# Kernel optimization log

Hardware: AMD Instinct MI355X
Metric: run time of the kernel (lower is better)

## Reference

```python
import jax, jax.numpy as jnp
import numpy as np

V, D, H, L, F, S, B = 32000, 1024, 16, 6, 4096, 1024, 2
DK = D // H
SCALE = float(np.sqrt(DK))
NEG = -1e9


def _make_pe(max_len, d_model):
    pos = np.arange(max_len, dtype=np.float32)[:, None]
    div = np.exp(np.arange(0, d_model, 2, dtype=np.float32) * (-np.log(10000.0) / d_model))
    pe = np.zeros((max_len, d_model), dtype=np.float32)
    pe[:, 0::2] = np.sin(pos * div)
    pe[:, 1::2] = np.cos(pos * div)
    return jnp.asarray(pe)


def _ln(x, g, b, eps=1e-5):
    m = x.mean(-1, keepdims=True)
    v = ((x - m) ** 2).mean(-1, keepdims=True)
    return (x - m) / jnp.sqrt(v + eps) * g + b


def setup_inputs() -> dict:
    key = jax.random.key(0)
    ks = jax.random.split(key, 10)
    std = 0.02
    tokens = jax.random.randint(ks[0], (B, S), 0, V)
    emb = (jax.random.normal(ks[1], (V, D)) * std).at[0].set(0.0)  # padding_idx=0 row zeroed
    pe = _make_pe(4096, D)
    Wq = jax.random.normal(ks[2], (L, D, D)) * std
    Wk = jax.random.normal(ks[3], (L, D, D)) * std
    Wv = jax.random.normal(ks[4], (L, D, D)) * std
    Wo = jax.random.normal(ks[5], (L, D, D)) * std
    bo = jnp.zeros((L, D))
    g1 = jnp.ones((L, D)); be1 = jnp.zeros((L, D))
    g2 = jnp.ones((L, D)); be2 = jnp.zeros((L, D))
    W1 = jax.random.normal(ks[6], (L, D, F)) * std
    b1 = jnp.zeros((L, F))
    W2 = jax.random.normal(ks[7], (L, F, D)) * std
    b2 = jnp.zeros((L, D))
    gf = jnp.ones((D,)); bf = jnp.zeros((D,))
    Wout = jax.random.normal(ks[8], (D, V)) * std
    bout = jnp.zeros((V,))
    return dict(tokens=tokens, emb=emb, pe=pe, Wq=Wq, Wk=Wk, Wv=Wv, Wo=Wo, bo=bo,
                g1=g1, be1=be1, g2=g2, be2=be2, W1=W1, b1=b1, W2=W2, b2=b2,
                gf=gf, bf=bf, Wout=Wout, bout=bout)


def reference(tokens, emb, pe, Wq, Wk, Wv, Wo, bo, g1, be1, g2, be2,
              W1, b1, W2, b2, gf, bf, Wout, bout):
    Bx, Sx = tokens.shape
    x = emb[tokens] * jnp.sqrt(jnp.float32(D)) + pe[:Sx]  # (B,S,D)
    pad = tokens == 0  # (B,S) padding mask
    causal = jnp.triu(jnp.ones((Sx, Sx), dtype=bool), 1)
    mask = causal[None, None] | pad[:, None, None, :]  # (B,1,S,S), True = masked
    for l in range(L):
        h = _ln(x, g1[l], be1[l])
        q = (h @ Wq[l]).reshape(Bx, Sx, H, DK)
        k = (h @ Wk[l]).reshape(Bx, Sx, H, DK)
        v = (h @ Wv[l]).reshape(Bx, Sx, H, DK)
        scores = jnp.einsum('bqhd,bkhd->bhqk', q, k) / SCALE
        scores = jnp.where(mask, NEG, scores)  # masked_fill(mask, -1e9)
        a = jax.nn.softmax(scores, axis=-1)
        ctx = jnp.einsum('bhqk,bkhd->bqhd', a, v).reshape(Bx, Sx, D)
        x = x + ctx @ Wo[l] + bo[l]
        h = _ln(x, g2[l], be2[l])
        x = x + jax.nn.gelu(h @ W1[l] + b1[l], approximate=False) @ W2[l] + b2[l]
    x = _ln(x, gf, bf)
    return x @ Wout + bout  # (B,S,V)
```

## Files before the change

kernel.cpp:

```cpp
#include <hip/hip_runtime.h>
#include <hip/hip_bf16.h>
#include <stdint.h>

typedef __hip_bfloat16 bf16;
typedef __attribute__((ext_vector_type(8))) short bf16x8;
typedef __attribute__((ext_vector_type(4))) float f32x4;

#define DEV static __device__ __forceinline__

DEV float b2f(bf16 v) { return __bfloat162float(v); }
DEV bf16  f2b(float v) { return __float2bfloat16(v); }

DEV void gload16(const void* g, void* l) {
  __builtin_amdgcn_global_load_lds(
      (__attribute__((address_space(1))) void*)(void*)g,
      (__attribute__((address_space(3))) void*)l, 16, 0, 0);
}

DEV f32x4 mfma16(bf16x8 a, bf16x8 b, f32x4 c) {
  return __builtin_amdgcn_mfma_f32_16x16x32_bf16(a, b, c, 0, 0, 0);
}

__global__ __launch_bounds__(256) void embed_kernel(
    const int* __restrict__ tok, const float* __restrict__ emb,
    const float* __restrict__ pe, float* __restrict__ x)
{
  const int r = blockIdx.x, t = threadIdx.x;
  const int s = r & 1023;
  const int tk = tok[r];
  const int d = t * 4;
  const float* ep = emb + (size_t)tk * 1024 + d;
  const float* pp = pe + (size_t)s * 1024 + d;
  float* xp = x + (size_t)r * 1024 + d;
  #pragma unroll
  for (int j = 0; j < 4; ++j)
    xp[j] = ep[j] * 32.0f + pp[j];
}

__global__ __launch_bounds__(256) void ln_kernel(
    const float* __restrict__ x, const float* __restrict__ g,
    const float* __restrict__ be, bf16* __restrict__ h)
{
  const int r = blockIdx.x, t = threadIdx.x;
  const float4 v = ((const float4*)(x + (size_t)r * 1024))[t];
  float s  = v.x + v.y + v.z + v.w;
  float sq = v.x * v.x + v.y * v.y + v.z * v.z + v.w * v.w;
  #pragma unroll
  for (int d = 1; d < 64; d <<= 1) {
    s  += __shfl_xor(s, d);
    sq += __shfl_xor(sq, d);
  }
  __shared__ float red[8];
  const int w = t >> 6, l = t & 63;
  if (l == 0) { red[w] = s; red[4 + w] = sq; }
  __syncthreads();
  s  = red[0] + red[1] + red[2] + red[3];
  sq = red[4] + red[5] + red[6] + red[7];
  const float mean = s * (1.0f / 1024.0f);
  const float var  = sq * (1.0f / 1024.0f) - mean * mean;
  const float inv  = 1.0f / sqrtf(var + 1e-5f);
  bf16* hp = h + (size_t)r * 1024 + t * 4;
  const float* gp = g + t * 4;
  const float* bp = be + t * 4;
  const float vv[4] = {v.x, v.y, v.z, v.w};
  #pragma unroll
  for (int j = 0; j < 4; ++j)
    hp[j] = f2b((vv[j] - mean) * inv * gp[j] + bp[j]);
}

__global__ __launch_bounds__(256) void ln_res_kernel(
    float* __restrict__ x, const float* __restrict__ P, int np,
    const float* __restrict__ bias, const float* __restrict__ g,
    const float* __restrict__ be, bf16* __restrict__ h)
{
  const int r = blockIdx.x, t = threadIdx.x;
  float4 v = ((const float4*)(x + (size_t)r * 1024))[t];
  for (int i = 0; i < np; ++i) {
    const float4 pv = ((const float4*)(P + ((size_t)i * 2048 + r) * 1024))[t];
    v.x += pv.x; v.y += pv.y; v.z += pv.z; v.w += pv.w;
  }
  const float4 bv = ((const float4*)bias)[t];
  v.x += bv.x; v.y += bv.y; v.z += bv.z; v.w += bv.w;

  float s  = v.x + v.y + v.z + v.w;
  float sq = v.x * v.x + v.y * v.y + v.z * v.z + v.w * v.w;
  #pragma unroll
  for (int d = 1; d < 64; d <<= 1) {
    s  += __shfl_xor(s, d);
    sq += __shfl_xor(sq, d);
  }
  __shared__ float red[8];
  const int w = t >> 6, l = t & 63;
  if (l == 0) { red[w] = s; red[4 + w] = sq; }
  __syncthreads();
  s  = red[0] + red[1] + red[2] + red[3];
  sq = red[4] + red[5] + red[6] + red[7];
  const float mean = s * (1.0f / 1024.0f);
  const float var  = sq * (1.0f / 1024.0f) - mean * mean;
  const float inv  = 1.0f / sqrtf(var + 1e-5f);

  ((float4*)(x + (size_t)r * 1024))[t] = v;
  bf16* hp = h + (size_t)r * 1024 + t * 4;
  const float* gp = g + t * 4;
  const float* bp = be + t * 4;
  const float vv[4] = {v.x, v.y, v.z, v.w};
  #pragma unroll
  for (int j = 0; j < 4; ++j)
    hp[j] = f2b((vv[j] - mean) * inv * gp[j] + bp[j]);
}

DEV void transpose_tile(const float* __restrict__ in, bf16* __restrict__ out,
                        int ldin, int ldout, int r0, int c0, int t)
{
  __shared__ bf16 tile[64][64];
  #pragma unroll
  for (int i = 0; i < 4; ++i) {
    const int r = i * 16 + (t >> 4), c = (t & 15) * 4;
    const float4 v = *(const float4*)&in[(size_t)(r0 + r) * ldin + c0 + c];
    tile[r][c + 0] = f2b(v.x);
    tile[r][c + 1] = f2b(v.y);
    tile[r][c + 2] = f2b(v.z);
    tile[r][c + 3] = f2b(v.w);
  }
  __syncthreads();
  #pragma unroll
  for (int i = 0; i < 2; ++i) {
    const int oc = i * 32 + (t >> 3);
    const int rr = (t & 7) * 8;
    unsigned short tmp[8] __attribute__((aligned(16)));
    #pragma unroll
    for (int j = 0; j < 8; ++j)
      tmp[j] = ((const unsigned short*)tile)[(rr + j) * 64 + oc];
    *(uint4*)&out[(size_t)(c0 + oc) * ldout + r0 + rr] = *(const uint4*)tmp;
  }
}

__global__ __launch_bounds__(256) void transpose_cast_kernel(
    const float* __restrict__ in, bf16* __restrict__ out, int ldin, int ldout)
{
  transpose_tile(in, out, ldin, ldout, blockIdx.y * 64, blockIdx.x * 64, threadIdx.x);
}

DEV void prep_dispatch(int wid,
    const float* Wq, const float* Wk, const float* Wv, const float* Wo,
    const float* W1, const float* W2,
    bf16* WqkvT, bf16* WoT, bf16* W1T, bf16* W2T, int t)
{
  const float* src; bf16* dst; int ldin, ldout, tx, ty;
  if (wid < 768) {
    const int m = wid >> 8, tt = wid & 255;
    src = (m == 0) ? Wq : (m == 1) ? Wk : Wv;
    dst = WqkvT + (size_t)m * 1024 * 1024;
    ldin = 1024; ldout = 1024; tx = tt & 15; ty = tt >> 4;
  } else if (wid < 1024) {
    const int tt = wid - 768;
    src = Wo; dst = WoT; ldin = 1024; ldout = 1024; tx = tt & 15; ty = tt >> 4;
  } else if (wid < 2048) {
    const int tt = wid - 1024;
    src = W1; dst = W1T; ldin = 4096; ldout = 1024; tx = tt & 63; ty = tt >> 6;
  } else {
    const int tt = wid - 2048;
    src = W2; dst = W2T; ldin = 1024; ldout = 4096; tx = tt & 15; ty = tt >> 4;
  }
  transpose_tile(src, dst, ldin, ldout, ty * 64, tx * 64, t);
}

__global__ __launch_bounds__(256) void prep_layer_kernel(
    const float* __restrict__ Wq, const float* __restrict__ Wk,
    const float* __restrict__ Wv, const float* __restrict__ Wo,
    const float* __restrict__ W1, const float* __restrict__ W2,
    bf16* __restrict__ WqkvT, bf16* __restrict__ WoT,
    bf16* __restrict__ W1T, bf16* __restrict__ W2T)
{
  prep_dispatch(blockIdx.x, Wq, Wk, Wv, Wo, W1, W2,
                WqkvT, WoT, W1T, W2T, threadIdx.x);
}

__global__ __launch_bounds__(256) void prep_all_kernel(
    const float* __restrict__ Wq, const float* __restrict__ Wk,
    const float* __restrict__ Wv, const float* __restrict__ Wo,
    const float* __restrict__ W1, const float* __restrict__ W2,
    bf16* __restrict__ WqkvT, bf16* __restrict__ WoT,
    bf16* __restrict__ W1T, bf16* __restrict__ W2T)
{
  const int layer = blockIdx.x / 3072;
  const int wid = blockIdx.x - layer * 3072;
  const size_t DD = (size_t)1024 * 1024, DF = (size_t)1024 * 4096;
  prep_dispatch(wid,
      Wq + layer * DD, Wk + layer * DD, Wv + layer * DD, Wo + layer * DD,
      W1 + layer * DF, W2 + layer * DF,
      WqkvT + layer * 3 * DD, WoT + layer * DD,
      W1T + layer * DF, W2T + layer * DF, threadIdx.x);
}

__global__ __launch_bounds__(256) void transpose_v_kernel(
    const bf16* __restrict__ qkv, bf16* __restrict__ vT)
{
  __shared__ bf16 tile[64][64];
  const int t = threadIdx.x;
  const int s0 = blockIdx.x * 64;
  const int bh = blockIdx.y;
  const int b = bh >> 4, h = bh & 15;
  const bf16* in = qkv + (size_t)(b * 1024) * 3072 + 2048 + h * 64;
  #pragma unroll
  for (int i = 0; i < 2; ++i) {
    const int r = i * 32 + (t >> 3), c = (t & 7) * 8;
    *(uint4*)&tile[r][c] = *(const uint4*)&in[(size_t)(s0 + r) * 3072 + c];
  }
  __syncthreads();
  bf16* out = vT + (size_t)(bh * 64) * 1024;
  #pragma unroll
  for (int i = 0; i < 2; ++i) {
    const int oc = i * 32 + (t >> 3);
    const int rr = (t & 7) * 8;
    unsigned short tmp[8] __attribute__((aligned(16)));
    #pragma unroll
    for (int j = 0; j < 8; ++j)
      tmp[j] = ((const unsigned short*)tile)[(rr + j) * 64 + oc];
    *(uint4*)&out[(size_t)oc * 1024 + s0 + rr] = *(const uint4*)tmp;
  }
}

template<int EPI, int BM, int SWZ>
__global__ __launch_bounds__(256) void gemm_pl(
    const bf16* __restrict__ A, int lda,
    const bf16* __restrict__ BT, int ldb,
    void* __restrict__ Cp, int ldc,
    const float* __restrict__ bias,
    int ksl)
{
  constexpr int ABUF = BM * 32;
  constexpr int MR = BM / 32;
  __shared__ bf16 As[3 * ABUF];
  __shared__ bf16 Bs[3 * 4096];
  const int t = threadIdx.x;

  int bm, bn;
  if constexpr (SWZ) {
    const int nbm = gridDim.x;
    const int nwg = nbm * gridDim.y;
    int wid = blockIdx.x + nbm * blockIdx.y;
    wid = (wid & 7) * (nwg >> 3) + (wid >> 3);
    bm = wid % nbm; bn = wid / nbm;
  } else {
    bm = blockIdx.x; bn = blockIdx.y;
  }

  const int w = t >> 6, l = t & 63;
  const int wr = (w >> 1) * (BM / 2), wc = (w & 1) * 64;
  const int l15 = l & 15, l4 = l >> 4;
  const int kbeg = blockIdx.z * ksl;
  const int ntiles = ksl >> 5;

  const int colblk = (((t & 3) ^ ((t >> 3) & 3))) * 8;
  const bf16* gA = A  + (size_t)(bm * BM  + (t >> 2)) * lda + colblk + kbeg;
  const bf16* gB = BT + (size_t)(bn * 128 + (t >> 2)) * ldb + colblk + kbeg;
  bf16* lA = As + w * 512;
  bf16* lB = Bs + w * 512;

  auto stage = [&](int tile, int buf) {
    const int k0 = tile * 32;
    gload16(gA + k0, lA + buf * ABUF);
    if constexpr (BM == 128)
      gload16(gA + (size_t)64 * lda + k0, lA + buf * ABUF + 2048);
    gload16(gB + k0, lB + buf * 4096);
    gload16(gB + (size_t)64 * ldb + k0, lB + buf * 4096 + 2048);
  };

  f32x4 acc[MR][4];
  #pragma unroll
  for (int m = 0; m < MR; ++m)
    #pragma unroll
    for (int n = 0; n < 4; ++n)
      acc[m][n] = (f32x4){0.f, 0.f, 0.f, 0.f};

  stage(0, 0);
  stage(1, 1);

  const int rdcol = ((l4 ^ ((l15 >> 1) & 3))) * 8;

  int buf = 0;
  for (int kt = 0; kt < ntiles; ++kt) {
    if (kt + 2 < ntiles) {
      int pb = buf + 2; if (pb >= 3) pb -= 3;
      stage(kt + 2, pb);
      __builtin_amdgcn_sched_barrier(0);
      if constexpr (BM == 128) asm volatile("s_waitcnt vmcnt(8)" ::: "memory");
      else                     asm volatile("s_waitcnt vmcnt(6)" ::: "memory");
    } else if (kt + 1 < ntiles) {
      if constexpr (BM == 128) asm volatile("s_waitcnt vmcnt(4)" ::: "memory");
      else                     asm volatile("s_waitcnt vmcnt(3)" ::: "memory");
    } else {
      asm volatile("s_waitcnt vmcnt(0)" ::: "memory");
    }
    __builtin_amdgcn_s_barrier();
    __builtin_amdgcn_sched_barrier(0);

    const bf16* Ab = As + buf * ABUF;
    const bf16* Bb = Bs + buf * 4096;
    bf16x8 af[MR], bfr[4];
    #pragma unroll
    for (int m = 0; m < MR; ++m)
      af[m] = *(const bf16x8*)&Ab[(wr + m * 16 + l15) * 32 + rdcol];
    #pragma unroll
    for (int n = 0; n < 4; ++n)
      bfr[n] = *(const bf16x8*)&Bb[(wc + n * 16 + l15) * 32 + rdcol];
    #pragma unroll
    for (int m = 0; m < MR; ++m)
      #pragma unroll
      for (int n = 0; n < 4; ++n)
        acc[m][n] = mfma16(af[m], bfr[n], acc[m][n]);

    __builtin_amdgcn_sched_barrier(0);
    __builtin_amdgcn_s_barrier();
    if (++buf >= 3) buf = 0;
  }

  const int crow = bm * BM + wr, ccol = bn * 128 + wc;
  #pragma unroll
  for (int n = 0; n < 4; ++n) {
    const int col = ccol + n * 16 + l15;
    float bv = 0.f;
    if (EPI == 1 || EPI == 2) bv = bias[col];
    #pragma unroll
    for (int m = 0; m < MR; ++m) {
      const int row = crow + m * 16 + l4 * 4;
      #pragma unroll
      for (int r = 0; r < 4; ++r) {
        const float v = acc[m][n][r];
        if (EPI == 0) {
          ((bf16*)Cp)[(size_t)(row + r) * ldc + col] = f2b(v);
        } else if (EPI == 1) {
          ((float*)Cp)[(size_t)(row + r) * ldc + col] = v + bv;
        } else if (EPI == 2) {
          const float u = v + bv;
          const float gel = 0.5f * u * (1.0f + erff(u * 0.70710678118654752f));
          ((bf16*)Cp)[(size_t)(row + r) * ldc + col] = f2b(gel);
        } else {
          const int M = gridDim.x * BM;
          ((float*)Cp)[((size_t)blockIdx.z * M + row + r) * ldc + col] = v;
        }
      }
    }
  }
}

__global__ __launch_bounds__(512, 2) void gemm256(
    const bf16* __restrict__ A, int lda,
    const bf16* __restrict__ BT, int ldb,
    float* __restrict__ C, int ldc,
    const float* __restrict__ bias, int K)
{
  __shared__ bf16 As[2][16384];
  __shared__ bf16 Bs[2][16384];
  const int t = threadIdx.x;

  const int nbm = gridDim.x;
  const int nwg = nbm * gridDim.y;
  int wid = blockIdx.x + nbm * blockIdx.y;
  wid = (wid & 7) * (nwg >> 3) + (wid >> 3);
  const int bm = wid % nbm, bn = wid / nbm;

  const int w = t >> 6, l = t & 63;
  const int wm = w >> 2, wn = w & 3;
  const int l15 = l & 15, l4 = l >> 4;

  const int scol = ((t & 7) ^ ((t >> 3) & 7)) * 8;
  const bf16* gA = A  + (size_t)(bm * 256 + (t >> 3)) * lda + scol;
  const bf16* gB = BT + (size_t)(bn * 256 + (t >> 3)) * ldb + scol;
  const int ldst = w * 512;

  auto stage = [&](int kt, int buf) {
    const int k0 = kt * 64;
    #pragma unroll
    for (int i = 0; i < 4; ++i)
      gload16(gA + (size_t)(i * 64) * lda + k0, &As[buf][i * 4096 + ldst]);
    #pragma unroll
    for (int i = 0; i < 4; ++i)
      gload16(gB + (size_t)(i * 64) * ldb + k0, &Bs[buf][i * 4096 + ldst]);
  };

  f32x4 acc[8][4];
  #pragma unroll
  for (int m = 0; m < 8; ++m)
    #pragma unroll
    for (int n = 0; n < 4; ++n)
      acc[m][n] = (f32x4){0.f, 0.f, 0.f, 0.f};

  const int NT = K >> 6;
  stage(0, 0);

  const int arow = wm * 128 + l15;
  const int brow = wn * 64 + l15;

  for (int kt = 0; kt < NT; ++kt) {
    const int buf = kt & 1;
    if (kt + 1 < NT) {
      stage(kt + 1, buf ^ 1);
      __builtin_amdgcn_sched_barrier(0);
      asm volatile("s_waitcnt vmcnt(8)" ::: "memory");
    } else {
      asm volatile("s_waitcnt vmcnt(0)" ::: "memory");
    }
    __builtin_amdgcn_s_barrier();
    __builtin_amdgcn_sched_barrier(0);

    #pragma unroll
    for (int ks = 0; ks < 2; ++ks) {
      const int csw = ((ks * 4 + l4) ^ (l15 & 7)) * 8;
      bf16x8 af[8], bfr[4];
      #pragma unroll
      for (int m = 0; m < 8; ++m)
        af[m] = *(const bf16x8*)&As[buf][(arow + m * 16) * 64 + csw];
      #pragma unroll
      for (int n = 0; n < 4; ++n)
        bfr[n] = *(const bf16x8*)&Bs[buf][(brow + n * 16) * 64 + csw];
      __builtin_amdgcn_s_setprio(1);
      #pragma unroll
      for (int m = 0; m < 8; ++m)
        #pragma unroll
        for (int n = 0; n < 4; ++n)
          acc[m][n] = mfma16(af[m], bfr[n], acc[m][n]);
      __builtin_amdgcn_s_setprio(0);
    }

    __builtin_amdgcn_sched_barrier(0);
    __builtin_amdgcn_s_barrier();
  }

  #pragma unroll
  for (int n = 0; n < 4; ++n) {
    const int col = bn * 256 + wn * 64 + n * 16 + l15;
    const float bv = bias[col];
    #pragma unroll
    for (int m = 0; m < 8; ++m) {
      const int row = bm * 256 + wm * 128 + m * 16 + l4 * 4;
      #pragma unroll
      for (int r = 0; r < 4; ++r)
        C[(size_t)(row + r) * ldc + col] = acc[m][n][r] + bv;
    }
  }
}

__global__ __launch_bounds__(256) void attn_kernel(
    const bf16* __restrict__ qkv, const bf16* __restrict__ vT,
    const int* __restrict__ tokens, bf16* __restrict__ ctx)
{
  __shared__ bf16 Ks[128 * 64];
  __shared__ bf16 VTs[64 * 128];
  __shared__ bf16 Ps[128 * 128];

  const int qt = blockIdx.x;
  const int bh = blockIdx.y;
  const int b = bh >> 4, h = bh & 15;
  const int t = threadIdx.x, w = t >> 6, l = t & 63;
  const int l15 = l & 15, l4 = l >> 4;
  const int q0 = qt * 128;

  bf16x8 aq[2][2];
  #pragma unroll
  for (int m = 0; m < 2; ++m)
    #pragma unroll
    for (int ks = 0; ks < 2; ++ks)
      aq[m][ks] = *(const bf16x8*)(qkv +
          (size_t)(b * 1024 + q0 + w * 32 + m * 16 + l15) * 3072 +
          h * 64 + ks * 32 + l4 * 8);

  f32x4 o[2][4];
  float m_run[2][4], l_run[2][4];
  #pragma unroll
  for (int m = 0; m < 2; ++m)
    #pragma unroll
    for (int r = 0; r < 4; ++r) { m_run[m][r] = -1e30f; l_run[m][r] = 0.f; }
  #pragma unroll
  for (int m = 0; m < 2; ++m)
    #pragma unroll
    for (int nn = 0; nn < 4; ++nn)
      o[m][nn] = (f32x4){0.f, 0.f, 0.f, 0.f};

  const bf16* kb = qkv + (size_t)(b * 1024) * 3072 + 1024 + h * 64;
  const bf16* vb = vT + (size_t)(bh * 64) * 1024;
  const int* tb = tokens + b * 1024;

  const int kSrcCol = ((t & 7) ^ ((t >> 3) & 7)) * 8;
  const int vSrcCol = ((t & 15) ^ (t >> 4)) * 8;

  for (int jt = 0; jt <= qt; ++jt) {
    const int j0 = jt * 128;
    __syncthreads();
    #pragma unroll
    for (int i = 0; i < 4; ++i)
      gload16(kb + (size_t)(j0 + i * 32 + (t >> 3)) * 3072 + kSrcCol,
              Ks + i * 2048 + w * 512);
    #pragma unroll
    for (int i = 0; i < 4; ++i)
      gload16(vb + (size_t)(i * 16 + (t >> 4)) * 1024 + j0 + vSrcCol,
              VTs + i * 2048 + w * 512);
    __syncthreads();

    f32x4 s[2][8];
    #pragma unroll
    for (int m = 0; m < 2; ++m)
      #pragma unroll
      for (int n = 0; n < 8; ++n)
        s[m][n] = (f32x4){0.f, 0.f, 0.f, 0.f};
    #pragma unroll
    for (int ks = 0; ks < 2; ++ks) {
      #pragma unroll
      for (int n = 0; n < 8; ++n) {
        const bf16x8 bk = *(const bf16x8*)
            &Ks[(n * 16 + l15) * 64 + ((ks * 32 + l4 * 8) ^ ((l15 & 7) * 8))];
        #pragma unroll
        for (int m = 0; m < 2; ++m)
          s[m][n] = mfma16(aq[m][ks], bk, s[m][n]);
      }
    }

    float padv[8];
    #pragma unroll
    for (int n = 0; n < 8; ++n)
      padv[n] = (tb[j0 + n * 16 + l15] == 0) ? 1.f : 0.f;

    #pragma unroll
    for (int m = 0; m < 2; ++m) {
      #pragma unroll
      for (int r = 0; r < 4; ++r) {
        const int rloc = l4 * 4 + r;
        const int qrow = q0 + w * 32 + m * 16 + rloc;
        float vals[8];
        float mx = -1e30f;
        #pragma unroll
        for (int n = 0; n < 8; ++n) {
          const int jg = j0 + n * 16 + l15;
          float v = s[m][n][r] * 0.125f;
          if (jg > qrow || padv[n] != 0.f) v = -1e9f;
          vals[n] = v;
          mx = fmaxf(mx, v);
        }
        #pragma unroll
        for (int d = 1; d < 16; d <<= 1) mx = fmaxf(mx, __shfl_xor(mx, d));
        const float newm = fmaxf(m_run[m][r], mx);
        const float sc = __expf(m_run[m][r] - newm);
        m_run[m][r] = newm;
        float rs = 0.f;
        #pragma unroll
        for (int n = 0; n < 8; ++n) {
          const float pv = __expf(vals[n] - newm);
          vals[n] = pv;
          rs += pv;
        }
        #pragma unroll
        for (int d = 1; d < 16; d <<= 1) rs += __shfl_xor(rs, d);
        l_run[m][r] = l_run[m][r] * sc + rs;
        #pragma unroll
        for (int nn = 0; nn < 4; ++nn) o[m][nn][r] = o[m][nn][r] * sc;
        #pragma unroll
        for (int n = 0; n < 8; ++n)
          Ps[(w * 32 + m * 16 + rloc) * 128 +
             ((n * 16 + l15) ^ (rloc * 8))] = f2b(vals[n]);
      }
    }
    __syncthreads();

    #pragma unroll
    for (int ks = 0; ks < 4; ++ks) {
      bf16x8 ap[2];
      #pragma unroll
      for (int m = 0; m < 2; ++m)
        ap[m] = *(const bf16x8*)
            &Ps[(w * 32 + m * 16 + l15) * 128 + ((ks * 32 + l4 * 8) ^ (l15 * 8))];
      #pragma unroll
      for (int nn = 0; nn < 4; ++nn) {
        const bf16x8 bv = *(const bf16x8*)
            &VTs[(nn * 16 + l15) * 128 + ((ks * 32 + l4 * 8) ^ (l15 * 8))];
        #pragma unroll
        for (int m = 0; m < 2; ++m)
          o[m][nn] = mfma16(ap[m], bv, o[m][nn]);
      }
    }
  }

  #pragma unroll
  for (int m = 0; m < 2; ++m) {
    #pragma unroll
    for (int r = 0; r < 4; ++r) {
      const float inv = 1.0f / l_run[m][r];
      const int qrow = q0 + w * 32 + m * 16 + l4 * 4 + r;
      #pragma unroll
      for (int nn = 0; nn < 4; ++nn)
        ctx[(size_t)(b * 1024 + qrow) * 1024 + h * 64 + nn * 16 + l15] =
            f2b(o[m][nn][r] * inv);
    }
  }
}

__global__ __launch_bounds__(64) void attn_fixup_kernel(
    const int* __restrict__ tokens, const bf16* __restrict__ vT,
    bf16* __restrict__ ctx)
{
  const int bh = blockIdx.x;
  const int b = bh >> 4, h = bh & 15;
  __shared__ int p0s;
  if (threadIdx.x == 0) {
    int p = 0;
    const int* tb = tokens + b * 1024;
    while (p < 1024 && tb[p] == 0) ++p;
    p0s = p;
  }
  __syncthreads();
  const int P0 = p0s;
  if (P0 == 0) return;
  const int dk = threadIdx.x;
  const bf16* vrow = vT + (size_t)(bh * 64 + dk) * 1024;
  float sum = 0.f;
  for (int sIdx = 0; sIdx < 1024; ++sIdx) sum += b2f(vrow[sIdx]);
  const bf16 mv = f2b(sum * (1.0f / 1024.0f));
  for (int q = 0; q < P0; ++q)
    ctx[(size_t)(b * 1024 + q) * 1024 + h * 64 + dk] = mv;
}

extern "C" void kernel_launch(void* const* d_in, const int* in_sizes, int n_in,
                              void* d_out, int out_size, void* d_ws, size_t ws_size,
                              hipStream_t stream)
{
  (void)in_sizes; (void)n_in; (void)out_size;
  const int*   tokens = (const int*)d_in[0];
  const float* emb  = (const float*)d_in[1];
  const float* pe   = (const float*)d_in[2];
  const float* Wq   = (const float*)d_in[3];
  const float* Wk   = (const float*)d_in[4];
  const float* Wv   = (const float*)d_in[5];
  const float* Wo   = (const float*)d_in[6];
  const float* bo   = (const float*)d_in[7];
  const float* g1   = (const float*)d_in[8];
  const float* be1  = (const float*)d_in[9];
  const float* g2   = (const float*)d_in[10];
  const float* be2  = (const float*)d_in[11];
  const float* W1   = (const float*)d_in[12];
  const float* b1   = (const float*)d_in[13];
  const float* W2   = (const float*)d_in[14];
  const float* b2   = (const float*)d_in[15];
  const float* gf   = (const float*)d_in[16];
  const float* bff  = (const float*)d_in[17];
  const float* Wout = (const float*)d_in[18];
  const float* bout = (const float*)d_in[19];
  float* out = (float*)d_out;

  char* p = (char*)d_ws;
  auto alloc = [&](size_t bytes) {
    char* q = p;
    p += (bytes + 255) & ~(size_t)255;
    return q;
  };
  float* x    = (float*)alloc((size_t)2048 * 1024 * 4);
  float* Pp   = (float*)alloc((size_t)4 * 2048 * 1024 * 4);
  bf16* h     = (bf16*)alloc((size_t)2048 * 1024 * 2);
  bf16* qkv   = (bf16*)alloc((size_t)2048 * 3072 * 2);
  bf16* vT    = (bf16*)alloc((size_t)2048 * 1024 * 2);
  bf16* ctx   = (bf16*)alloc((size_t)2048 * 1024 * 2);
  bf16* ff    = (bf16*)alloc((size_t)2048 * 4096 * 2);
  bf16* WoutT = (bf16*)alloc((size_t)32000 * 1024 * 2);

  const size_t DD = (size_t)1024 * 1024;
  const size_t DF = (size_t)1024 * 4096;

  const size_t perLayerW = (3 * DD + DD + DF + DF) * 2;
  const size_t used = (size_t)(p - (char*)d_ws);
  const bool fullprep = ws_size >= used + 6 * perLayerW + 8192;
  const int NL = fullprep ? 6 : 1;
  bf16* WqkvT = (bf16*)alloc((size_t)NL * 3 * DD * 2);
  bf16* WoT   = (bf16*)alloc((size_t)NL * DD * 2);
  bf16* W1T   = (bf16*)alloc((size_t)NL * DF * 2);
  bf16* W2T   = (bf16*)alloc((size_t)NL * DF * 2);

  if (fullprep)
    prep_all_kernel<<<6 * 3072, 256, 0, stream>>>(
        Wq, Wk, Wv, Wo, W1, W2, WqkvT, WoT, W1T, W2T);

  embed_kernel<<<2048, 256, 0, stream>>>(tokens, emb, pe, x);

  for (int l = 0; l < 6; ++l) {
    const bf16* wqkvt; const bf16* wot; const bf16* w1t; const bf16* w2t;
    if (fullprep) {
      wqkvt = WqkvT + (size_t)l * 3 * DD;
      wot   = WoT   + (size_t)l * DD;
      w1t   = W1T   + (size_t)l * DF;
      w2t   = W2T   + (size_t)l * DF;
    } else {
      prep_layer_kernel<<<3072, 256, 0, stream>>>(
          Wq + l * DD, Wk + l * DD, Wv + l * DD, Wo + l * DD,
          W1 + l * DF, W2 + l * DF, WqkvT, WoT, W1T, W2T);
      wqkvt = WqkvT; wot = WoT; w1t = W1T; w2t = W2T;
    }

    if (l == 0)
      ln_kernel<<<2048, 256, 0, stream>>>(x, g1, be1, h);
    else
      ln_res_kernel<<<2048, 256, 0, stream>>>(
          x, Pp, 4, b2 + (l - 1) * 1024, g1 + l * 1024, be1 + l * 1024, h);

    gemm_pl<0, 64, 0><<<dim3(32, 24, 1), 256, 0, stream>>>(
        h, 1024, wqkvt, 1024, qkv, 3072, (const float*)nullptr, 1024);
    transpose_v_kernel<<<dim3(16, 32), 256, 0, stream>>>(qkv, vT);
    attn_kernel<<<dim3(8, 32), 256, 0, stream>>>(qkv, vT, tokens, ctx);
    attn_fixup_kernel<<<32, 64, 0, stream>>>(tokens, vT, ctx);
    gemm_pl<3, 64, 0><<<dim3(32, 8, 2), 256, 0, stream>>>(
        ctx, 1024, wot, 1024, Pp, 1024, (const float*)nullptr, 512);
    ln_res_kernel<<<2048, 256, 0, stream>>>(
        x, Pp, 2, bo + l * 1024, g2 + l * 1024, be2 + l * 1024, h);
    gemm_pl<2, 128, 0><<<dim3(16, 32, 1), 256, 0, stream>>>(
        h, 1024, w1t, 1024, ff, 4096, b1 + l * 4096, 1024);
    gemm_pl<3, 128, 0><<<dim3(16, 8, 4), 256, 0, stream>>>(
        ff, 4096, w2t, 4096, Pp, 1024, (const float*)nullptr, 1024);
  }

  ln_res_kernel<<<2048, 256, 0, stream>>>(x, Pp, 4, b2 + 5 * 1024, gf, bff, h);
  transpose_cast_kernel<<<dim3(500, 16), 256, 0, stream>>>(Wout, WoutT, 32000, 1024);
  gemm256<<<dim3(8, 125), 512, 0, stream>>>(
      h, 1024, WoutT, 1024, out, 32000, bout, 1024);
}
```

Baseline: 1.493 ms.

## Triple-buffer gemm256 with BK=32 and interleave A/B prefetch between MFMA halves

Rewrites the 256x256 GEMM main loop so it uses three LDS stages of K=32 in place of two stages of K=64, keeping two tiles in flight. Each iteration splits its MFMA work into two halves, and the A and B loads for stage kt+2 are issued between the halves so global traffic overlaps compute. The LDS swizzle changes to match the 32-wide rows. This adds an extra barrier per iteration and halves the K per iteration, which may raise sync overhead relative to compute.

```diff
diff --git a/kernel.cpp b/kernel.cpp
--- a/kernel.cpp
+++ b/kernel.cpp
@@ -351,8 +351,8 @@
     float* __restrict__ C, int ldc,
     const float* __restrict__ bias, int K)
 {
-  __shared__ bf16 As[2][16384];
-  __shared__ bf16 Bs[2][16384];
+  __shared__ bf16 As[3][8192];
+  __shared__ bf16 Bs[3][8192];
   const int t = threadIdx.x;
 
   const int nbm = gridDim.x;
@@ -365,20 +365,14 @@
   const int wm = w >> 2, wn = w & 3;
   const int l15 = l & 15, l4 = l >> 4;
 
-  const int scol = ((t & 7) ^ ((t >> 3) & 7)) * 8;
-  const bf16* gA = A  + (size_t)(bm * 256 + (t >> 3)) * lda + scol;
-  const bf16* gB = BT + (size_t)(bn * 256 + (t >> 3)) * ldb + scol;
-  const int ldst = w * 512;
-
-  auto stage = [&](int kt, int buf) {
-    const int k0 = kt * 64;
-    #pragma unroll
-    for (int i = 0; i < 4; ++i)
-      gload16(gA + (size_t)(i * 64) * lda + k0, &As[buf][i * 4096 + ldst]);
-    #pragma unroll
-    for (int i = 0; i < 4; ++i)
-      gload16(gB + (size_t)(i * 64) * ldb + k0, &Bs[buf][i * 4096 + ldst]);
-  };
+  const int colblk = ((t & 3) ^ ((t >> 3) & 3)) * 8;
+  const bf16* gA = A  + (size_t)(bm * 256 + (t >> 2)) * lda + colblk;
+  const bf16* gB = BT + (size_t)(bn * 256 + (t >> 2)) * ldb + colblk;
+  const int dst = w * 512;
+
+  const int rd = (l4 ^ ((l15 >> 1) & 3)) * 8;
+  const int arow = wm * 128 + l15;
+  const int brow = wn * 64 + l15;
 
   f32x4 acc[8][4];
   #pragma unroll
@@ -387,45 +381,70 @@
     for (int n = 0; n < 4; ++n)
       acc[m][n] = (f32x4){0.f, 0.f, 0.f, 0.f};
 
-  const int NT = K >> 6;
-  stage(0, 0);
-
-  const int arow = wm * 128 + l15;
-  const int brow = wn * 64 + l15;
-
+  const int NT = K >> 5;
+
+  auto stageA = [&](int kt, int buf) {
+    const int k0 = kt * 32;
+    gload16(gA + k0, &As[buf][dst]);
+    gload16(gA + (size_t)128 * lda + k0, &As[buf][4096 + dst]);
+  };
+  auto stageB = [&](int kt, int buf) {
+    const int k0 = kt * 32;
+    gload16(gB + k0, &Bs[buf][dst]);
+    gload16(gB + (size_t)128 * ldb + k0, &Bs[buf][4096 + dst]);
+  };
+
+  stageA(0, 0); stageB(0, 0);
+  stageA(1, 1); stageB(1, 1);
+
+  int buf = 0;
   for (int kt = 0; kt < NT; ++kt) {
-    const int buf = kt & 1;
-    if (kt + 1 < NT) {
-      stage(kt + 1, buf ^ 1);
-      __builtin_amdgcn_sched_barrier(0);
-      asm volatile("s_waitcnt vmcnt(8)" ::: "memory");
-    } else {
-      asm volatile("s_waitcnt vmcnt(0)" ::: "memory");
-    }
+    if (kt + 1 < NT) asm volatile("s_waitcnt vmcnt(4)" ::: "memory");
+    else             asm volatile("s_waitcnt vmcnt(0)" ::: "memory");
     __builtin_amdgcn_s_barrier();
     __builtin_amdgcn_sched_barrier(0);
 
-    #pragma unroll
-    for (int ks = 0; ks < 2; ++ks) {
-      const int csw = ((ks * 4 + l4) ^ (l15 & 7)) * 8;
-      bf16x8 af[8], bfr[4];
-      #pragma unroll
-      for (int m = 0; m < 8; ++m)
-        af[m] = *(const bf16x8*)&As[buf][(arow + m * 16) * 64 + csw];
+    int pb = buf + 2; if (pb >= 3) pb -= 3;
+    const bf16* Ab = As[buf];
+    const bf16* Bb = Bs[buf];
+
+    bf16x8 bfr[4], af[4];
+    #pragma unroll
+    for (int n = 0; n < 4; ++n)
+      bfr[n] = *(const bf16x8*)&Bb[(brow + n * 16) * 32 + rd];
+    #pragma unroll
+    for (int m = 0; m < 4; ++m)
+      af[m] = *(const bf16x8*)&Ab[(arow + m * 16) * 32 + rd];
+    if (kt + 2 < NT) stageA(kt + 2, pb);
+    asm volatile("s_waitcnt lgkmcnt(0)" ::: "memory");
+    __builtin_amdgcn_sched_barrier(0);
+    __builtin_amdgcn_s_setprio(1);
+    #pragma unroll
+    for (int m = 0; m < 4; ++m)
       #pragma unroll
       for (int n = 0; n < 4; ++n)
-        bfr[n] = *(const bf16x8*)&Bs[buf][(brow + n * 16) * 64 + csw];
-      __builtin_amdgcn_s_setprio(1);
-      #pragma unroll
-      for (int m = 0; m < 8; ++m)
-        #pragma unroll
-        for (int n = 0; n < 4; ++n)
-          acc[m][n] = mfma16(af[m], bfr[n], acc[m][n]);
-      __builtin_amdgcn_s_setprio(0);
-    }
-
+        acc[m][n] = mfma16(af[m], bfr[n], acc[m][n]);
+    __builtin_amdgcn_s_setprio(0);
     __builtin_amdgcn_sched_barrier(0);
     __builtin_amdgcn_s_barrier();
+
+    #pragma unroll
+    for (int m = 0; m < 4; ++m)
+      af[m] = *(const bf16x8*)&Ab[(arow + (m + 4) * 16) * 32 + rd];
+    if (kt + 2 < NT) stageB(kt + 2, pb);
+    asm volatile("s_waitcnt lgkmcnt(0)" ::: "memory");
+    __builtin_amdgcn_sched_barrier(0);
+    __builtin_amdgcn_s_setprio(1);
+    #pragma unroll
+    for (int m = 0; m < 4; ++m)
+      #pragma unroll
+      for (int n = 0; n < 4; ++n)
+        acc[m + 4][n] = mfma16(af[m], bfr[n], acc[m + 4][n]);
+    __builtin_amdgcn_s_setprio(0);
+    __builtin_amdgcn_sched_barrier(0);
+    __builtin_amdgcn_s_barrier();
+
+    if (++buf >= 3) buf = 0;
   }
 
   #pragma unroll
```

After: 1.475 ms. About the same (-1.2%).
